# Kernel tuning notes

Hardware: AMD Instinct MI355X
Metric: run time of the kernel (lower is better)

The kernel has to match this reference:

```python
import jax, jax.numpy as jnp
import numpy as np

N_HEADS = 16
EPS = 1e-5

def _ln(x, g, b):
    m = jnp.mean(x, -1, keepdims=True)
    v = jnp.mean((x - m) ** 2, -1, keepdims=True)
    return (x - m) / jnp.sqrt(v + EPS) * g + b

def _split(x):
    B, S, D = x.shape
    return x.reshape(B, S, N_HEADS, D // N_HEADS).transpose(0, 2, 1, 3)

def _merge(x):
    B, H, S, d = x.shape
    return x.transpose(0, 2, 1, 3).reshape(B, S, H * d)

def _sdpa(q, k, v, mask=None):
    scale = 1.0 / jnp.sqrt(jnp.asarray(q.shape[-1], q.dtype))
    s = jnp.einsum('bhqd,bhkd->bhqk', q, k) * scale
    if mask is not None:
        s = s + mask
    return jnp.einsum('bhqk,bhkd->bhqd', jax.nn.softmax(s, axis=-1), v)

def setup_inputs() -> dict:
    key = jax.random.key(0)
    ks = jax.random.split(key, 20)
    B, T, D = 2, 2048, 1024
    NC, K, NL = 32, 2, 128
    DFF = 4 * D
    w = lambda k, shp: (jax.random.normal(k, shp, jnp.float32) * 0.02)
    return {
        'x': jax.random.normal(ks[0], (B, T, D), jnp.float32),
        'neighbors': jax.random.normal(ks[1], (B, NC, K, NL, D), jnp.float32),
        'sa_ln_g': jnp.ones((D,), jnp.float32), 'sa_ln_b': jnp.zeros((D,), jnp.float32),
        'sa_wq': w(ks[2], (D, D)), 'sa_wk': w(ks[3], (D, D)),
        'sa_wv': w(ks[4], (D, D)), 'sa_wo': w(ks[5], (D, D)),
        'cca_lnq_g': jnp.ones((D,), jnp.float32), 'cca_lnq_b': jnp.zeros((D,), jnp.float32),
        'cca_lnkv_g': jnp.ones((D,), jnp.float32), 'cca_lnkv_b': jnp.zeros((D,), jnp.float32),
        'cca_wq': w(ks[6], (D, D)), 'cca_wk': w(ks[7], (D, D)),
        'cca_wv': w(ks[8], (D, D)), 'cca_wo': w(ks[9], (D, D)),
        'ffn_ln_g': jnp.ones((D,), jnp.float32), 'ffn_ln_b': jnp.zeros((D,), jnp.float32),
        'ffn_w1': w(ks[10], (D, DFF)), 'ffn_w2': w(ks[11], (DFF, D)),
        'chunk_size': 64,
    }

def reference(x, neighbors, sa_ln_g, sa_ln_b, sa_wq, sa_wk, sa_wv, sa_wo,
              cca_lnq_g, cca_lnq_b, cca_lnkv_g, cca_lnkv_b,
              cca_wq, cca_wk, cca_wv, cca_wo,
              ffn_ln_g, ffn_ln_b, ffn_w1, ffn_w2, chunk_size):
    B, T, D = x.shape
    # --- causal self-attention (pre-norm, residual) ---
    h = _ln(x, sa_ln_g, sa_ln_b)
    q, k, v = _split(h @ sa_wq), _split(h @ sa_wk), _split(h @ sa_wv)
    mask = jnp.triu(jnp.full((T, T), -jnp.inf, x.dtype), 1)
    x = x + _merge(_sdpa(q, k, v, mask)) @ sa_wo
    # --- cross-chunk attention ---
    Bn, NC, K, NL, _ = neighbors.shape
    E = neighbors.reshape(B * NC, K * NL, D)
    padded_T = NC * chunk_size
    if T < padded_T:
        xc = jnp.concatenate([x, jnp.zeros((B, padded_T - T, D), x.dtype)], axis=1)
    else:
        xc = x[:, :padded_T, :]
    Hc = xc.reshape(B * NC, chunk_size, D)
    qn = _ln(Hc, cca_lnq_g, cca_lnq_b)
    kvn = _ln(E, cca_lnkv_g, cca_lnkv_b)
    qh = _split(qn @ cca_wq)
    kh = _split(kvn @ cca_wk)
    vh = _split(kvn @ cca_wv)
    cca = _merge(_sdpa(qh, kh, vh)) @ cca_wo
    cca = cca.reshape(B, padded_T, D)[:, :T, :]
    x = x + cca
    # --- FFN (pre-norm, residual) ---
    h = _ln(x, ffn_ln_g, ffn_ln_b)
    return x + jax.nn.gelu(h @ ffn_w1, approximate=False) @ ffn_w2
```

## Files before the change

### kernel.cpp

```cpp
#include <hip/hip_runtime.h>
#include <math.h>

typedef __attribute__((ext_vector_type(8))) short bf16x8;
typedef __attribute__((ext_vector_type(4))) float f32x4;

#define MFMA(a, b, c) __builtin_amdgcn_mfma_f32_16x16x32_bf16((a), (b), (c), 0, 0, 0)

__device__ __forceinline__ unsigned short f2bf(float f) {
  union { float f; unsigned int u; } v; v.f = f;
  unsigned int r = v.u + 0x7fffu + ((v.u >> 16) & 1u);
  return (unsigned short)(r >> 16);
}

typedef __attribute__((address_space(1))) const void* as1cv;
typedef __attribute__((address_space(3))) void* as3v;
__device__ __forceinline__ void gl_lds16(const void* g, void* l) {
  __builtin_amdgcn_global_load_lds((as1cv)g, (as3v)l, 16, 0, 0);
}

__global__ __launch_bounds__(256) void ln_bf16(
    const float* __restrict__ in, const float* __restrict__ gw,
    const float* __restrict__ bw, unsigned short* __restrict__ out) {
  int row = blockIdx.x;
  const float4* rp = (const float4*)(in + (size_t)row * 1024);
  float4 v = rp[threadIdx.x];
  float s = v.x + v.y + v.z + v.w;
  float ss = v.x * v.x + v.y * v.y + v.z * v.z + v.w * v.w;
#pragma unroll
  for (int o = 32; o; o >>= 1) {
    s += __shfl_down(s, o);
    ss += __shfl_down(ss, o);
  }
  __shared__ float red[10];
  int lane = threadIdx.x & 63, wid = threadIdx.x >> 6;
  if (lane == 0) { red[wid] = s; red[4 + wid] = ss; }
  __syncthreads();
  if (threadIdx.x == 0) {
    float ts = red[0] + red[1] + red[2] + red[3];
    float tss = red[4] + red[5] + red[6] + red[7];
    float mean = ts * (1.0f / 1024.0f);
    float var = tss * (1.0f / 1024.0f) - mean * mean;
    red[8] = mean;
    red[9] = rsqrtf(var + 1e-5f);
  }
  __syncthreads();
  float mean = red[8], rstd = red[9];
  float4 g = ((const float4*)gw)[threadIdx.x];
  float4 b = ((const float4*)bw)[threadIdx.x];
  ushort4 o;
  o.x = f2bf((v.x - mean) * rstd * g.x + b.x);
  o.y = f2bf((v.y - mean) * rstd * g.y + b.y);
  o.z = f2bf((v.z - mean) * rstd * g.z + b.z);
  o.w = f2bf((v.w - mean) * rstd * g.w + b.w);
  ((ushort4*)(out + (size_t)row * 1024))[threadIdx.x] = o;
}

__global__ __launch_bounds__(256) void wtrans(
    const float* __restrict__ W, unsigned short* __restrict__ Wt, int K, int N) {
  __shared__ float Ts[32][33];
  int n0 = blockIdx.x * 32, k0 = blockIdx.y * 32;
  int ry = threadIdx.x >> 3, cx = (threadIdx.x & 7) * 4;
  float4 v = *(const float4*)(W + (size_t)(k0 + ry) * N + n0 + cx);
  Ts[ry][cx + 0] = v.x; Ts[ry][cx + 1] = v.y;
  Ts[ry][cx + 2] = v.z; Ts[ry][cx + 3] = v.w;
  __syncthreads();
  ushort4 o;
  o.x = f2bf(Ts[cx + 0][ry]); o.y = f2bf(Ts[cx + 1][ry]);
  o.z = f2bf(Ts[cx + 2][ry]); o.w = f2bf(Ts[cx + 3][ry]);
  *(ushort4*)(Wt + (size_t)(n0 + ry) * K + k0 + cx) = o;
}

template <int EPI>
__global__ __launch_bounds__(256) void gemm_bt(
    const unsigned short* __restrict__ A, const unsigned short* __restrict__ Bt,
    const float* __restrict__ R, void* __restrict__ Cv,
    int M, int N, int K, int rowOff, int Tkv) {
  __shared__ unsigned short As[128 * 32];
  __shared__ unsigned short Bs[128 * 32];
  const int tid = threadIdx.x;
  const int lane = tid & 63, w = tid >> 6;
  const int wr = w >> 1, wc = w & 1;
  const int lr = lane & 15, kb = lane >> 4;
  const int bn = blockIdx.x, bm = blockIdx.y;

  const int sRow = w * 16 + (lane >> 2);
  const int sCol = (lane & 3) * 8;
  const unsigned short* gA0 = A + (size_t)(bm * 128 + sRow) * K + sCol;
  const unsigned short* gA1 = gA0 + (size_t)64 * K;
  const unsigned short* gB0 = Bt + (size_t)(bn * 128 + sRow) * K + sCol;
  const unsigned short* gB1 = gB0 + (size_t)64 * K;
  unsigned short* lA0 = As + w * 512;
  unsigned short* lA1 = As + 2048 + w * 512;
  unsigned short* lB0 = Bs + w * 512;
  unsigned short* lB1 = Bs + 2048 + w * 512;

  const f32x4 z4 = {0.f, 0.f, 0.f, 0.f};
  f32x4 acc[4][4];
#pragma unroll
  for (int m = 0; m < 4; ++m)
#pragma unroll
    for (int n = 0; n < 4; ++n) acc[m][n] = z4;

  for (int k0 = 0; k0 < K; k0 += 32) {
    gl_lds16(gA0 + k0, lA0);
    gl_lds16(gA1 + k0, lA1);
    gl_lds16(gB0 + k0, lB0);
    gl_lds16(gB1 + k0, lB1);
    __syncthreads();
    bf16x8 aF[4], bF[4];
#pragma unroll
    for (int m = 0; m < 4; ++m)
      aF[m] = *(const bf16x8*)&As[(wr * 64 + m * 16 + lr) * 32 + kb * 8];
#pragma unroll
    for (int n = 0; n < 4; ++n)
      bF[n] = *(const bf16x8*)&Bs[(wc * 64 + n * 16 + lr) * 32 + kb * 8];
#pragma unroll
    for (int m = 0; m < 4; ++m)
#pragma unroll
      for (int n = 0; n < 4; ++n) acc[m][n] = MFMA(aF[m], bF[n], acc[m][n]);
    __syncthreads();
  }

#pragma unroll
  for (int m = 0; m < 4; ++m) {
    int row0 = bm * 128 + wr * 64 + m * 16 + kb * 4;
#pragma unroll
    for (int n = 0; n < 4; ++n) {
      int col = bn * 128 + wc * 64 + n * 16 + lr;
      f32x4 a = acc[m][n];
      if (EPI == 0 || EPI == 2) {
        unsigned short* C = (unsigned short*)Cv;
#pragma unroll
        for (int r = 0; r < 4; ++r) {
          float v = a[r];
          if (EPI == 2) v = 0.5f * v * (1.0f + erff(v * 0.70710678118654752f));
          C[(size_t)(row0 + r) * N + col] = f2bf(v);
        }
      } else if (EPI == 1) {
        float* C = (float*)Cv;
#pragma unroll
        for (int r = 0; r < 4; ++r)
          C[(size_t)(row0 + r) * N + col] =
              a.s0 * 0.0f + a[r] + R[(size_t)(row0 + r) * N + col];
      } else {
        unsigned short* C = (unsigned short*)Cv;
        int grow = rowOff + row0;
        int batch = grow / Tkv;
        int p = grow - batch * Tkv;
        int hh = col >> 6, d = col & 63;
        ushort4 st;
        st.x = f2bf(a[0]); st.y = f2bf(a[1]);
        st.z = f2bf(a[2]); st.w = f2bf(a[3]);
        *(ushort4*)&C[(((size_t)batch * 16 + hh) * 64 + d) * Tkv + p] = st;
      }
    }
  }
}

template <bool CAUSAL>
__global__ __launch_bounds__(256) void attn_mfma(
    const unsigned short* __restrict__ Q, const unsigned short* __restrict__ K,
    const unsigned short* __restrict__ Vt, unsigned short* __restrict__ O,
    int Tq, int Tkv) {
  __shared__ unsigned short Ps[4 * 16 * 64];
  const int tid = threadIdx.x, lane = tid & 63, w = tid >> 6;
  const int lr = lane & 15, kb = lane >> 4;
  const int qt = blockIdx.x, h = blockIdx.y, z = blockIdx.z;

  const unsigned short* Qp =
      Q + ((size_t)z * Tq + qt * 64 + w * 16 + lr) * 1024 + h * 64;
  bf16x8 qf0 = *(const bf16x8*)(Qp + kb * 8);
  bf16x8 qf1 = *(const bf16x8*)(Qp + 32 + kb * 8);
  const unsigned short* Kb = K + (size_t)z * Tkv * 1024 + h * 64;
  const unsigned short* Vb = Vt + (size_t)(z * 16 + h) * 64 * Tkv;
  char* PsB = (char*)Ps + w * 2048;

  const f32x4 z4 = {0.f, 0.f, 0.f, 0.f};
  float m_[4] = {-INFINITY, -INFINITY, -INFINITY, -INFINITY};
  float l_[4] = {0.f, 0.f, 0.f, 0.f};
  f32x4 oacc[4];
#pragma unroll
  for (int n = 0; n < 4; ++n) oacc[n] = z4;

  const int ktMax = CAUSAL ? qt : (Tkv >> 6) - 1;
  for (int kt = 0; kt <= ktMax; ++kt) {
    f32x4 sac[4];
#pragma unroll
    for (int f = 0; f < 4; ++f) sac[f] = z4;
#pragma unroll
    for (int f = 0; f < 4; ++f) {
      const unsigned short* kp = Kb + (size_t)(kt * 64 + f * 16 + lr) * 1024;
      bf16x8 kf0 = *(const bf16x8*)(kp + kb * 8);
      bf16x8 kf1 = *(const bf16x8*)(kp + 32 + kb * 8);
      sac[f] = MFMA(qf0, kf0, sac[f]);
      sac[f] = MFMA(qf1, kf1, sac[f]);
    }
    float alpha[4], mn[4], rs[4];
#pragma unroll
    for (int r = 0; r < 4; ++r) {
      float t = -3e38f;
#pragma unroll
      for (int f = 0; f < 4; ++f) {
        float v = sac[f][r] * 0.125f;
        if (CAUSAL && kt == qt) {
          if (f * 16 + lr > w * 16 + kb * 4 + r) v = -3e38f;
        }
        sac[f][r] = v;
        t = fmaxf(t, v);
      }
      t = fmaxf(t, __shfl_xor(t, 1));
      t = fmaxf(t, __shfl_xor(t, 2));
      t = fmaxf(t, __shfl_xor(t, 4));
      t = fmaxf(t, __shfl_xor(t, 8));
      mn[r] = fmaxf(m_[r], t);
      alpha[r] = __expf(m_[r] - mn[r]);
      m_[r] = mn[r];
      rs[r] = 0.f;
    }
#pragma unroll
    for (int f = 0; f < 4; ++f) {
#pragma unroll
      for (int r = 0; r < 4; ++r) {
        float p = __expf(sac[f][r] - mn[r]);
        rs[r] += p;
        int q = kb * 4 + r, kv = f * 16 + lr;
        int byte = (q * 128 + kv * 2) ^ ((q & 7) << 4);
        *(unsigned short*)(PsB + byte) = f2bf(p);
      }
    }
#pragma unroll
    for (int r = 0; r < 4; ++r) {
      rs[r] += __shfl_xor(rs[r], 1);
      rs[r] += __shfl_xor(rs[r], 2);
      rs[r] += __shfl_xor(rs[r], 4);
      rs[r] += __shfl_xor(rs[r], 8);
      l_[r] = l_[r] * alpha[r] + rs[r];
    }
#pragma unroll
    for (int n = 0; n < 4; ++n) {
#pragma unroll
      for (int r = 0; r < 4; ++r) oacc[n][r] *= alpha[r];
    }
#pragma unroll
    for (int ks = 0; ks < 2; ++ks) {
      int byte = (lr * 128 + ks * 64 + kb * 16) ^ ((lr & 7) << 4);
      bf16x8 pf = *(const bf16x8*)(PsB + byte);
#pragma unroll
      for (int n = 0; n < 4; ++n) {
        const unsigned short* vp =
            Vb + (size_t)(n * 16 + lr) * Tkv + kt * 64 + ks * 32 + kb * 8;
        bf16x8 vf = *(const bf16x8*)vp;
        oacc[n] = MFMA(pf, vf, oacc[n]);
      }
    }
  }
  size_t orow0 = (size_t)z * Tq + qt * 64 + w * 16 + kb * 4;
#pragma unroll
  for (int r = 0; r < 4; ++r) {
    float inv = 1.0f / l_[r];
    unsigned short* op = O + (orow0 + r) * 1024 + h * 64;
#pragma unroll
    for (int n = 0; n < 4; ++n) op[n * 16 + lr] = f2bf(oacc[n][r] * inv);
  }
}

extern "C" void kernel_launch(void* const* d_in, const int* in_sizes, int n_in,
                              void* d_out, int out_size, void* d_ws,
                              size_t ws_size, hipStream_t stream) {
  const float* x = (const float*)d_in[0];
  const float* neigh = (const float*)d_in[1];
  const float* sa_ln_g = (const float*)d_in[2];
  const float* sa_ln_b = (const float*)d_in[3];
  const float* sa_wq = (const float*)d_in[4];
  const float* sa_wk = (const float*)d_in[5];
  const float* sa_wv = (const float*)d_in[6];
  const float* sa_wo = (const float*)d_in[7];
  const float* cca_lnq_g = (const float*)d_in[8];
  const float* cca_lnq_b = (const float*)d_in[9];
  const float* cca_lnkv_g = (const float*)d_in[10];
  const float* cca_lnkv_b = (const float*)d_in[11];
  const float* cca_wq = (const float*)d_in[12];
  const float* cca_wk = (const float*)d_in[13];
  const float* cca_wv = (const float*)d_in[14];
  const float* cca_wo = (const float*)d_in[15];
  const float* ffn_ln_g = (const float*)d_in[16];
  const float* ffn_ln_b = (const float*)d_in[17];
  const float* ffn_w1 = (const float*)d_in[18];
  const float* ffn_w2 = (const float*)d_in[19];
  float* out = (float*)d_out;

  char* wsb = (char*)d_ws;
  const size_t MB = 1024 * 1024;
  unsigned short* wqT = (unsigned short*)(wsb + 0 * MB);
  unsigned short* wkT = (unsigned short*)(wsb + 2 * MB);
  unsigned short* wvT = (unsigned short*)(wsb + 4 * MB);
  unsigned short* woT = (unsigned short*)(wsb + 6 * MB);
  unsigned short* cwqT = (unsigned short*)(wsb + 8 * MB);
  unsigned short* cwkT = (unsigned short*)(wsb + 10 * MB);
  unsigned short* cwvT = (unsigned short*)(wsb + 12 * MB);
  unsigned short* cwoT = (unsigned short*)(wsb + 14 * MB);
  unsigned short* w1T = (unsigned short*)(wsb + 16 * MB);
  unsigned short* w2T = (unsigned short*)(wsb + 24 * MB);
  float* X1 = (float*)(wsb + 32 * MB);
  float* X2 = (float*)(wsb + 48 * MB);
  unsigned short* CKH = (unsigned short*)(wsb + 64 * MB);
  unsigned short* CVT = (unsigned short*)(wsb + 96 * MB);
  unsigned short* A0 = (unsigned short*)(wsb + 128 * MB);
  unsigned short* QB = (unsigned short*)(wsb + 136 * MB);
  unsigned short* KB = (unsigned short*)(wsb + 144 * MB);
  unsigned short* VTs = (unsigned short*)(wsb + 152 * MB);
  unsigned short* AO = (unsigned short*)(wsb + 160 * MB);
  unsigned short* KVN = (unsigned short*)(wsb + 144 * MB);
  unsigned short* MID = CKH;

  dim3 blk(256);

  wtrans<<<dim3(32, 32), blk, 0, stream>>>(sa_wq, wqT, 1024, 1024);
  wtrans<<<dim3(32, 32), blk, 0, stream>>>(sa_wk, wkT, 1024, 1024);
  wtrans<<<dim3(32, 32), blk, 0, stream>>>(sa_wv, wvT, 1024, 1024);
  wtrans<<<dim3(32, 32), blk, 0, stream>>>(sa_wo, woT, 1024, 1024);
  wtrans<<<dim3(32, 32), blk, 0, stream>>>(cca_wq, cwqT, 1024, 1024);
  wtrans<<<dim3(32, 32), blk, 0, stream>>>(cca_wk, cwkT, 1024, 1024);
  wtrans<<<dim3(32, 32), blk, 0, stream>>>(cca_wv, cwvT, 1024, 1024);
  wtrans<<<dim3(32, 32), blk, 0, stream>>>(cca_wo, cwoT, 1024, 1024);
  wtrans<<<dim3(128, 32), blk, 0, stream>>>(ffn_w1, w1T, 1024, 4096);
  wtrans<<<dim3(32, 128), blk, 0, stream>>>(ffn_w2, w2T, 4096, 1024);

  ln_bf16<<<4096, blk, 0, stream>>>(x, sa_ln_g, sa_ln_b, A0);
  gemm_bt<0><<<dim3(8, 32), blk, 0, stream>>>(A0, wqT, nullptr, QB, 4096, 1024, 1024, 0, 0);
  gemm_bt<0><<<dim3(8, 32), blk, 0, stream>>>(A0, wkT, nullptr, KB, 4096, 1024, 1024, 0, 0);
  gemm_bt<3><<<dim3(8, 32), blk, 0, stream>>>(A0, wvT, nullptr, VTs, 4096, 1024, 1024, 0, 2048);
  attn_mfma<true><<<dim3(32, 16, 2), blk, 0, stream>>>(QB, KB, VTs, AO, 2048, 2048);
  gemm_bt<1><<<dim3(8, 32), blk, 0, stream>>>(AO, woT, x, X1, 4096, 1024, 1024, 0, 0);

  ln_bf16<<<4096, blk, 0, stream>>>(X1, cca_lnq_g, cca_lnq_b, A0);
  gemm_bt<0><<<dim3(8, 32), blk, 0, stream>>>(A0, cwqT, nullptr, QB, 4096, 1024, 1024, 0, 0);
  for (int half = 0; half < 2; ++half) {
    const float* nh = neigh + (size_t)half * 8192 * 1024;
    ln_bf16<<<8192, blk, 0, stream>>>(nh, cca_lnkv_g, cca_lnkv_b, KVN);
    gemm_bt<0><<<dim3(8, 64), blk, 0, stream>>>(
        KVN, cwkT, nullptr, CKH + (size_t)half * 8192 * 1024, 8192, 1024, 1024, 0, 0);
    gemm_bt<3><<<dim3(8, 64), blk, 0, stream>>>(
        KVN, cwvT, nullptr, CVT, 8192, 1024, 1024, half * 8192, 256);
  }
  attn_mfma<false><<<dim3(1, 16, 64), blk, 0, stream>>>(QB, CKH, CVT, AO, 64, 256);
  gemm_bt<1><<<dim3(8, 32), blk, 0, stream>>>(AO, cwoT, X1, X2, 4096, 1024, 1024, 0, 0);

  ln_bf16<<<4096, blk, 0, stream>>>(X2, ffn_ln_g, ffn_ln_b, A0);
  gemm_bt<2><<<dim3(32, 32), blk, 0, stream>>>(A0, w1T, nullptr, MID, 4096, 4096, 1024, 0, 0);
  gemm_bt<1><<<dim3(8, 32), blk, 0, stream>>>(MID, w2T, X2, out, 4096, 1024, 4096, 0, 0);
}
```

Measured before the change: 982.2 us.

## Fuse QKV and KV projection GEMMs and prefetch K/V tiles in attention

The separate Q, K and V projection GEMMs become one N=3072 GEMM, and the cross-attention K and V GEMMs become one N=2048 GEMM over all neighbors. A split epilogue writes row-major Q/K and the transposed V layout, which cuts launches and re-reads of the activation matrix. The attention kernel now preloads the next K tile and the current V fragments into registers before the MFMAs, pre-scales Q by 0.125 (exact in bf16), rotates causal query tiles across heads to balance load, and sets a min-blocks-per-CU launch bound. The cost is more register pressure, which may cause spills or lower occupancy, and a larger LN scratch buffer that now overlaps other workspace regions.

Result: faster. 954.4 us (-2.8%).

```diff
diff --git a/kernel.cpp b/kernel.cpp
--- a/kernel.cpp
+++ b/kernel.cpp
@@ -10,6 +10,10 @@
   union { float f; unsigned int u; } v; v.f = f;
   unsigned int r = v.u + 0x7fffu + ((v.u >> 16) & 1u);
   return (unsigned short)(r >> 16);
+}
+__device__ __forceinline__ float bf2f(unsigned short u) {
+  union { unsigned int u; float f; } v; v.u = ((unsigned int)u) << 16;
+  return v.f;
 }
 
 typedef __attribute__((address_space(1))) const void* as1cv;
@@ -74,7 +78,7 @@
 __global__ __launch_bounds__(256) void gemm_bt(
     const unsigned short* __restrict__ A, const unsigned short* __restrict__ Bt,
     const float* __restrict__ R, void* __restrict__ Cv,
-    int M, int N, int K, int rowOff, int Tkv) {
+    int M, int N, int K, int vSplit, int Tkv) {
   __shared__ unsigned short As[128 * 32];
   __shared__ unsigned short Bs[128 * 32];
   const int tid = threadIdx.x;
@@ -141,36 +145,53 @@
 #pragma unroll
         for (int r = 0; r < 4; ++r)
           C[(size_t)(row0 + r) * N + col] =
-              a.s0 * 0.0f + a[r] + R[(size_t)(row0 + r) * N + col];
+              a[r] + R[(size_t)(row0 + r) * N + col];
       } else {
-        unsigned short* C = (unsigned short*)Cv;
-        int grow = rowOff + row0;
-        int batch = grow / Tkv;
-        int p = grow - batch * Tkv;
-        int hh = col >> 6, d = col & 63;
-        ushort4 st;
-        st.x = f2bf(a[0]); st.y = f2bf(a[1]);
-        st.z = f2bf(a[2]); st.w = f2bf(a[3]);
-        *(ushort4*)&C[(((size_t)batch * 16 + hh) * 64 + d) * Tkv + p] = st;
+        if (col < vSplit) {
+          unsigned short* C =
+              (unsigned short*)Cv + (size_t)(col >> 10) * ((size_t)M << 10);
+          int cl = col & 1023;
+#pragma unroll
+          for (int r = 0; r < 4; ++r)
+            C[(size_t)(row0 + r) * 1024 + cl] = f2bf(a[r]);
+        } else {
+          unsigned short* Vb =
+              (unsigned short*)Cv + (size_t)(vSplit >> 10) * ((size_t)M << 10);
+          int cv = col - vSplit;
+          int hh = cv >> 6, d = cv & 63;
+          int batch = row0 / Tkv;
+          int p = row0 - batch * Tkv;
+          ushort4 st;
+          st.x = f2bf(a[0]); st.y = f2bf(a[1]);
+          st.z = f2bf(a[2]); st.w = f2bf(a[3]);
+          *(ushort4*)&Vb[(((size_t)batch * 16 + hh) * 64 + d) * Tkv + p] = st;
+        }
       }
     }
   }
 }
 
 template <bool CAUSAL>
-__global__ __launch_bounds__(256) void attn_mfma(
+__global__ __launch_bounds__(256, 4) void attn_mfma(
     const unsigned short* __restrict__ Q, const unsigned short* __restrict__ K,
     const unsigned short* __restrict__ Vt, unsigned short* __restrict__ O,
     int Tq, int Tkv) {
   __shared__ unsigned short Ps[4 * 16 * 64];
   const int tid = threadIdx.x, lane = tid & 63, w = tid >> 6;
   const int lr = lane & 15, kb = lane >> 4;
-  const int qt = blockIdx.x, h = blockIdx.y, z = blockIdx.z;
+  int qt = blockIdx.x;
+  if (CAUSAL) qt = (blockIdx.x + blockIdx.y) & 31;
+  const int h = blockIdx.y, z = blockIdx.z;
 
   const unsigned short* Qp =
       Q + ((size_t)z * Tq + qt * 64 + w * 16 + lr) * 1024 + h * 64;
   bf16x8 qf0 = *(const bf16x8*)(Qp + kb * 8);
   bf16x8 qf1 = *(const bf16x8*)(Qp + 32 + kb * 8);
+#pragma unroll
+  for (int j = 0; j < 8; ++j) {
+    qf0[j] = (short)f2bf(bf2f((unsigned short)qf0[j]) * 0.125f);
+    qf1[j] = (short)f2bf(bf2f((unsigned short)qf1[j]) * 0.125f);
+  }
   const unsigned short* Kb = K + (size_t)z * Tkv * 1024 + h * 64;
   const unsigned short* Vb = Vt + (size_t)(z * 16 + h) * 64 * Tkv;
   char* PsB = (char*)Ps + w * 2048;
@@ -183,25 +204,43 @@
   for (int n = 0; n < 4; ++n) oacc[n] = z4;
 
   const int ktMax = CAUSAL ? qt : (Tkv >> 6) - 1;
-  for (int kt = 0; kt <= ktMax; ++kt) {
-    f32x4 sac[4];
-#pragma unroll
-    for (int f = 0; f < 4; ++f) sac[f] = z4;
+
+  bf16x8 kf[8];
+  auto kload = [&](int kt) {
 #pragma unroll
     for (int f = 0; f < 4; ++f) {
       const unsigned short* kp = Kb + (size_t)(kt * 64 + f * 16 + lr) * 1024;
-      bf16x8 kf0 = *(const bf16x8*)(kp + kb * 8);
-      bf16x8 kf1 = *(const bf16x8*)(kp + 32 + kb * 8);
-      sac[f] = MFMA(qf0, kf0, sac[f]);
-      sac[f] = MFMA(qf1, kf1, sac[f]);
-    }
+      kf[f * 2 + 0] = *(const bf16x8*)(kp + kb * 8);
+      kf[f * 2 + 1] = *(const bf16x8*)(kp + 32 + kb * 8);
+    }
+  };
+  kload(0);
+
+  for (int kt = 0; kt <= ktMax; ++kt) {
+    bf16x8 vf[8];
+#pragma unroll
+    for (int ks = 0; ks < 2; ++ks)
+#pragma unroll
+      for (int n = 0; n < 4; ++n)
+        vf[ks * 4 + n] = *(const bf16x8*)(Vb + (size_t)(n * 16 + lr) * Tkv +
+                                          kt * 64 + ks * 32 + kb * 8);
+    f32x4 sac[4];
+#pragma unroll
+    for (int f = 0; f < 4; ++f) sac[f] = z4;
+#pragma unroll
+    for (int f = 0; f < 4; ++f) {
+      sac[f] = MFMA(qf0, kf[f * 2 + 0], sac[f]);
+      sac[f] = MFMA(qf1, kf[f * 2 + 1], sac[f]);
+    }
+    if (kt < ktMax) kload(kt + 1);
+
     float alpha[4], mn[4], rs[4];
 #pragma unroll
     for (int r = 0; r < 4; ++r) {
       float t = -3e38f;
 #pragma unroll
       for (int f = 0; f < 4; ++f) {
-        float v = sac[f][r] * 0.125f;
+        float v = sac[f][r];
         if (CAUSAL && kt == qt) {
           if (f * 16 + lr > w * 16 + kb * 4 + r) v = -3e38f;
         }
@@ -246,12 +285,7 @@
       int byte = (lr * 128 + ks * 64 + kb * 16) ^ ((lr & 7) << 4);
       bf16x8 pf = *(const bf16x8*)(PsB + byte);
 #pragma unroll
-      for (int n = 0; n < 4; ++n) {
-        const unsigned short* vp =
-            Vb + (size_t)(n * 16 + lr) * Tkv + kt * 64 + ks * 32 + kb * 8;
-        bf16x8 vf = *(const bf16x8*)vp;
-        oacc[n] = MFMA(pf, vf, oacc[n]);
-      }
+      for (int n = 0; n < 4; ++n) oacc[n] = MFMA(pf, vf[ks * 4 + n], oacc[n]);
     }
   }
   size_t orow0 = (size_t)z * Tq + qt * 64 + w * 16 + kb * 4;
@@ -291,13 +325,10 @@
 
   char* wsb = (char*)d_ws;
   const size_t MB = 1024 * 1024;
-  unsigned short* wqT = (unsigned short*)(wsb + 0 * MB);
-  unsigned short* wkT = (unsigned short*)(wsb + 2 * MB);
-  unsigned short* wvT = (unsigned short*)(wsb + 4 * MB);
+  unsigned short* wqkvT = (unsigned short*)(wsb + 0 * MB);
   unsigned short* woT = (unsigned short*)(wsb + 6 * MB);
   unsigned short* cwqT = (unsigned short*)(wsb + 8 * MB);
-  unsigned short* cwkT = (unsigned short*)(wsb + 10 * MB);
-  unsigned short* cwvT = (unsigned short*)(wsb + 12 * MB);
+  unsigned short* cwkvT = (unsigned short*)(wsb + 10 * MB);
   unsigned short* cwoT = (unsigned short*)(wsb + 14 * MB);
   unsigned short* w1T = (unsigned short*)(wsb + 16 * MB);
   unsigned short* w2T = (unsigned short*)(wsb + 24 * MB);
@@ -309,40 +340,34 @@
   unsigned short* QB = (unsigned short*)(wsb + 136 * MB);
   unsigned short* KB = (unsigned short*)(wsb + 144 * MB);
   unsigned short* VTs = (unsigned short*)(wsb + 152 * MB);
-  unsigned short* AO = (unsigned short*)(wsb + 160 * MB);
   unsigned short* KVN = (unsigned short*)(wsb + 144 * MB);
+  unsigned short* AO = (unsigned short*)(wsb + 168 * MB);
   unsigned short* MID = CKH;
 
   dim3 blk(256);
 
-  wtrans<<<dim3(32, 32), blk, 0, stream>>>(sa_wq, wqT, 1024, 1024);
-  wtrans<<<dim3(32, 32), blk, 0, stream>>>(sa_wk, wkT, 1024, 1024);
-  wtrans<<<dim3(32, 32), blk, 0, stream>>>(sa_wv, wvT, 1024, 1024);
+  wtrans<<<dim3(32, 32), blk, 0, stream>>>(sa_wq, wqkvT, 1024, 1024);
+  wtrans<<<dim3(32, 32), blk, 0, stream>>>(sa_wk, wqkvT + 1024 * 1024, 1024, 1024);
+  wtrans<<<dim3(32, 32), blk, 0, stream>>>(sa_wv, wqkvT + 2 * 1024 * 1024, 1024, 1024);
   wtrans<<<dim3(32, 32), blk, 0, stream>>>(sa_wo, woT, 1024, 1024);
   wtrans<<<dim3(32, 32), blk, 0, stream>>>(cca_wq, cwqT, 1024, 1024);
-  wtrans<<<dim3(32, 32), blk, 0, stream>>>(cca_wk, cwkT, 1024, 1024);
-  wtrans<<<dim3(32, 32), blk, 0, stream>>>(cca_wv, cwvT, 1024, 1024);
+  wtrans<<<dim3(32, 32), blk, 0, stream>>>(cca_wk, cwkvT, 1024, 1024);
+  wtrans<<<dim3(32, 32), blk, 0, stream>>>(cca_wv, cwkvT + 1024 * 1024, 1024, 1024);
   wtrans<<<dim3(32, 32), blk, 0, stream>>>(cca_wo, cwoT, 1024, 1024);
   wtrans<<<dim3(128, 32), blk, 0, stream>>>(ffn_w1, w1T, 1024, 4096);
   wtrans<<<dim3(32, 128), blk, 0, stream>>>(ffn_w2, w2T, 4096, 1024);
 
   ln_bf16<<<4096, blk, 0, stream>>>(x, sa_ln_g, sa_ln_b, A0);
-  gemm_bt<0><<<dim3(8, 32), blk, 0, stream>>>(A0, wqT, nullptr, QB, 4096, 1024, 1024, 0, 0);
-  gemm_bt<0><<<dim3(8, 32), blk, 0, stream>>>(A0, wkT, nullptr, KB, 4096, 1024, 1024, 0, 0);
-  gemm_bt<3><<<dim3(8, 32), blk, 0, stream>>>(A0, wvT, nullptr, VTs, 4096, 1024, 1024, 0, 2048);
+  gemm_bt<4><<<dim3(24, 32), blk, 0, stream>>>(A0, wqkvT, nullptr, QB, 4096,
+                                               3072, 1024, 2048, 2048);
   attn_mfma<true><<<dim3(32, 16, 2), blk, 0, stream>>>(QB, KB, VTs, AO, 2048, 2048);
   gemm_bt<1><<<dim3(8, 32), blk, 0, stream>>>(AO, woT, x, X1, 4096, 1024, 1024, 0, 0);
 
   ln_bf16<<<4096, blk, 0, stream>>>(X1, cca_lnq_g, cca_lnq_b, A0);
   gemm_bt<0><<<dim3(8, 32), blk, 0, stream>>>(A0, cwqT, nullptr, QB, 4096, 1024, 1024, 0, 0);
-  for (int half = 0; half < 2; ++half) {
-    const float* nh = neigh + (size_t)half * 8192 * 1024;
-    ln_bf16<<<8192, blk, 0, stream>>>(nh, cca_lnkv_g, cca_lnkv_b, KVN);
-    gemm_bt<0><<<dim3(8, 64), blk, 0, stream>>>(
-        KVN, cwkT, nullptr, CKH + (size_t)half * 8192 * 1024, 8192, 1024, 1024, 0, 0);
-    gemm_bt<3><<<dim3(8, 64), blk, 0, stream>>>(
-        KVN, cwvT, nullptr, CVT, 8192, 1024, 1024, half * 8192, 256);
-  }
+  ln_bf16<<<16384, blk, 0, stream>>>(neigh, cca_lnkv_g, cca_lnkv_b, KVN);
+  gemm_bt<4><<<dim3(16, 128), blk, 0, stream>>>(KVN, cwkvT, nullptr, CKH, 16384,
+                                                2048, 1024, 1024, 256);
   attn_mfma<false><<<dim3(1, 16, 64), blk, 0, stream>>>(QB, CKH, CVT, AO, 64, 256);
   gemm_bt<1><<<dim3(8, 32), blk, 0, stream>>>(AO, cwoT, X1, X2, 4096, 1024, 1024, 0, 0);
 
```
